# Optimization experiments

Hardware: AMD Instinct MI355X
Metric: run time of the kernel (lower is better)

## Reference

```python
import jax, jax.numpy as jnp
import numpy as np

N_NODES = 100000
N_EDGES = 1600000
IN_FEATS = 128
OUT_FEATS = 128


def setup_inputs() -> dict:
    key = jax.random.key(0)
    k1, k2, k3, k4, k5 = jax.random.split(key, 5)
    feature = jax.random.normal(k1, (N_NODES, IN_FEATS), dtype=jnp.float32)
    src = jax.random.randint(k2, (N_EDGES,), 0, N_NODES, dtype=jnp.int64)
    dst = jax.random.randint(k3, (N_EDGES,), 0, N_NODES, dtype=jnp.int64)
    # nn.Linear default init: U(-1/sqrt(in), 1/sqrt(in)); randn scaled is fine for a numeric baseline
    bound = 1.0 / np.sqrt(IN_FEATS)
    W = jax.random.uniform(k4, (OUT_FEATS, IN_FEATS), dtype=jnp.float32, minval=-bound, maxval=bound)
    b = jax.random.uniform(k5, (OUT_FEATS,), dtype=jnp.float32, minval=-bound, maxval=bound)
    return {"feature": feature, "src": src, "dst": dst, "W": W, "b": b}


def reference(feature, src, dst, W, b):
    # message passing: copy source feature along each edge, sum into destination node
    agg = jax.ops.segment_sum(feature[src], dst, num_segments=N_NODES)  # [N, in_feats]
    # node apply: ReLU(Linear(h))
    return jax.nn.relu(agg @ W.T + b)  # [N, out_feats]
```

## Files before the change

kernel.cpp:

```cpp
#include <hip/hip_runtime.h>

#define N_NODES 100000
#define N_EDGES 1600000
#define F 128

#define NB    1563
#define NBP2  2048
#define CAP   1280
#define CHUNK 8192

#define BIN_BLOCKS   196
#define HGEMM_BLOCKS 782
#define FRONT_GRID_LIN (BIN_BLOCKS + HGEMM_BLOCKS)

#define LDP  136
#define SMEM_BYTES 77824

typedef __bf16  bf16x8 __attribute__((ext_vector_type(8)));
typedef float   f32x4  __attribute__((ext_vector_type(4)));

__device__ inline unsigned short f32_to_bf16(float f) {
    unsigned u = __builtin_bit_cast(unsigned, f);
    u += 0x7FFFu + ((u >> 16) & 1u);
    return (unsigned short)(u >> 16);
}
__device__ inline unsigned pack_bf16x2(float lo, float hi) {
    return (unsigned)f32_to_bf16(lo) | ((unsigned)f32_to_bf16(hi) << 16);
}
__device__ inline void addrow(float* acc, const uint4 v) {
    acc[0] += __builtin_bit_cast(float, v.x << 16);
    acc[1] += __builtin_bit_cast(float, v.x & 0xFFFF0000u);
    acc[2] += __builtin_bit_cast(float, v.y << 16);
    acc[3] += __builtin_bit_cast(float, v.y & 0xFFFF0000u);
    acc[4] += __builtin_bit_cast(float, v.z << 16);
    acc[5] += __builtin_bit_cast(float, v.z & 0xFFFF0000u);
    acc[6] += __builtin_bit_cast(float, v.w << 16);
    acc[7] += __builtin_bit_cast(float, v.w & 0xFFFF0000u);
}

__global__ __launch_bounds__(1024) void gcn_front_lin(
    const float* __restrict__ feat, const float* __restrict__ W,
    const int* __restrict__ src, const int* __restrict__ dst,
    int* __restrict__ gcur, unsigned* __restrict__ bins,
    unsigned short* __restrict__ H)
{
    __shared__ __align__(16) unsigned char smem[SMEM_BYTES];

    const int tid = threadIdx.x;
    const int bx  = blockIdx.x;

    if (bx >= BIN_BLOCKS) {
        unsigned short* Alds = (unsigned short*)smem;
        unsigned short* Wlds = Alds + 128 * LDP;
        const int row0 = (bx - BIN_BLOCKS) * 128;

        #pragma unroll
        for (int i = 0; i < 4; ++i) {
            const int c = tid + i * 1024;
            const int r = c >> 5, cc = c & 31;
            const float4 v = *(const float4*)(W + (size_t)c * 4);
            uint2 p; p.x = pack_bf16x2(v.x, v.y); p.y = pack_bf16x2(v.z, v.w);
            *(uint2*)&Wlds[r * LDP + cc * 4] = p;
        }
        #pragma unroll
        for (int i = 0; i < 4; ++i) {
            const int c = tid + i * 1024;
            const int r = c >> 5, cc = c & 31;
            int gr = row0 + r; if (gr > N_NODES - 1) gr = N_NODES - 1;
            const float4 v = *(const float4*)(feat + (size_t)gr * F + cc * 4);
            uint2 p; p.x = pack_bf16x2(v.x, v.y); p.y = pack_bf16x2(v.z, v.w);
            *(uint2*)&Alds[r * LDP + cc * 4] = p;
        }
        __syncthreads();

        const int lane = tid & 63, wv = tid >> 6;
        const int lr = lane & 15, lq = lane >> 4;
        const int wr = wv & 7;
        const int wc = wv >> 3;

        f32x4 acc[4] = {};
        #pragma unroll
        for (int kk = 0; kk < 4; ++kk) {
            const bf16x8 a = __builtin_bit_cast(bf16x8,
                *(const uint4*)&Alds[(wr * 16 + lr) * LDP + kk * 32 + lq * 8]);
            #pragma unroll
            for (int n2 = 0; n2 < 4; ++n2) {
                const bf16x8 w = __builtin_bit_cast(bf16x8,
                    *(const uint4*)&Wlds[((wc * 4 + n2) * 16 + lr) * LDP + kk * 32 + lq * 8]);
                acc[n2] = __builtin_amdgcn_mfma_f32_16x16x32_bf16(a, w, acc[n2], 0, 0, 0);
            }
        }
        #pragma unroll
        for (int rg = 0; rg < 4; ++rg) {
            const int gr = row0 + wr * 16 + lq * 4 + rg;
            if (gr < N_NODES) {
                unsigned short* hrow = H + (size_t)gr * F;
                #pragma unroll
                for (int n2 = 0; n2 < 4; ++n2)
                    hrow[(wc * 4 + n2) * 16 + lr] = f32_to_bf16(acc[n2][rg]);
            }
        }
        return;
    }

    unsigned*       cnt    = (unsigned*)smem;
    unsigned*       off    = cnt + NBP2;
    int*            gbase  = (int*)(off + NBP2);
    unsigned*       staged = (unsigned*)(gbase + NBP2);
    unsigned short* sbk    = (unsigned short*)(staged + CHUNK);
    unsigned*       scan   = (unsigned*)(sbk + CHUNK);

    const int e0 = bx * CHUNK;

    #pragma unroll
    for (int i = 0; i < 2; ++i) cnt[tid + i * 1024] = 0;
    __syncthreads();

    int sv[8], dv[8];
    #pragma unroll
    for (int i = 0; i < 8; ++i) {
        const int e = e0 + tid + i * 1024;
        if (e < N_EDGES) {
            sv[i] = src[e];
            dv[i] = dst[e];
            atomicAdd(&cnt[dv[i] >> 6], 1u);
        } else dv[i] = -1;
    }
    __syncthreads();

    const unsigned s = cnt[2 * tid] + cnt[2 * tid + 1];
    scan[tid] = s;
    __syncthreads();
    for (int o = 1; o < 1024; o <<= 1) {
        const unsigned t = (tid >= o) ? scan[tid - o] : 0;
        __syncthreads();
        scan[tid] += t;
        __syncthreads();
    }
    const unsigned run = scan[tid] - s;
    off[2 * tid]     = run;
    off[2 * tid + 1] = run + cnt[2 * tid];
    __syncthreads();

    #pragma unroll
    for (int i = 0; i < 8; ++i) {
        if (dv[i] >= 0) {
            const int bk = dv[i] >> 6;
            const unsigned w = (unsigned)sv[i] | ((unsigned)(dv[i] & 63) << 17);
            const unsigned p = atomicAdd(&off[bk], 1u);
            staged[p] = w;
            sbk[p] = (unsigned short)bk;
        }
    }
    __syncthreads();

    #pragma unroll
    for (int i = 0; i < 2; ++i) {
        const int bk = 2 * tid + i;
        if (bk < NB && cnt[bk] > 0)
            gbase[bk] = atomicAdd(&gcur[bk], (int)cnt[bk]);
    }
    __syncthreads();

    const int c_tot = (int)scan[1023];
    for (int p = tid; p < c_tot; p += 1024) {
        const int bk = sbk[p];
        const int gp = gbase[bk] + (p - (int)(off[bk] - cnt[bk]));
        if (gp < CAP) bins[(size_t)bk * CAP + gp] = staged[p];
    }
}

__global__ __launch_bounds__(512) void gcn_accum_lin(
    const int* __restrict__ gcur,
    const unsigned* __restrict__ bins,
    const unsigned short* __restrict__ H,
    const float* __restrict__ b,
    float* __restrict__ out)
{
    __shared__ unsigned tmp[CAP];
    __shared__ unsigned list[CAP];
    __shared__ int cnt64[64], scn[64], pos64[64], cur64[64];

    const int tid = threadIdx.x;
    const int bkt = blockIdx.x;

    int c = gcur[bkt]; if (c > CAP) c = CAP;
    const unsigned* bb = bins + (size_t)bkt * CAP;

    for (int i = tid; i < c; i += 512) tmp[i] = bb[i];
    if (tid < 64) cnt64[tid] = 0;
    __syncthreads();

    for (int i = tid; i < c; i += 512) atomicAdd(&cnt64[(tmp[i] >> 17) & 63], 1);
    __syncthreads();

    if (tid < 64) scn[tid] = cnt64[tid];
    __syncthreads();
    #pragma unroll
    for (int o = 1; o < 64; o <<= 1) {
        int t = 0;
        if (tid < 64 && tid >= o) t = scn[tid - o];
        __syncthreads();
        if (tid < 64) scn[tid] += t;
        __syncthreads();
    }
    if (tid < 64) {
        const int st = scn[tid] - cnt64[tid];
        pos64[tid] = st;
        cur64[tid] = st;
    }
    __syncthreads();

    for (int i = tid; i < c; i += 512) {
        const unsigned w = tmp[i];
        const int p = atomicAdd(&cur64[(w >> 17) & 63], 1);
        list[p] = w;
    }
    __syncthreads();

    const int grp = tid >> 4;
    const int sl  = tid & 15;
    const int n0  = bkt * 64;

    #pragma unroll
    for (int ni = 0; ni < 2; ++ni) {
        const int l  = grp * 2 + ni;
        const int st = pos64[l];
        const int en = st + cnt64[l];

        float a0[8] = {0,0,0,0,0,0,0,0};
        float a1[8] = {0,0,0,0,0,0,0,0};
        int k = st;
        for (; k + 7 < en; k += 8) {
            const unsigned w0 = list[k],     w1 = list[k + 1];
            const unsigned w2 = list[k + 2], w3 = list[k + 3];
            const unsigned w4 = list[k + 4], w5 = list[k + 5];
            const unsigned w6 = list[k + 6], w7 = list[k + 7];
            const uint4 v0 = *(const uint4*)(H + (size_t)(w0 & 0x1FFFF) * F + sl * 8);
            const uint4 v1 = *(const uint4*)(H + (size_t)(w1 & 0x1FFFF) * F + sl * 8);
            const uint4 v2 = *(const uint4*)(H + (size_t)(w2 & 0x1FFFF) * F + sl * 8);
            const uint4 v3 = *(const uint4*)(H + (size_t)(w3 & 0x1FFFF) * F + sl * 8);
            const uint4 v4 = *(const uint4*)(H + (size_t)(w4 & 0x1FFFF) * F + sl * 8);
            const uint4 v5 = *(const uint4*)(H + (size_t)(w5 & 0x1FFFF) * F + sl * 8);
            const uint4 v6 = *(const uint4*)(H + (size_t)(w6 & 0x1FFFF) * F + sl * 8);
            const uint4 v7 = *(const uint4*)(H + (size_t)(w7 & 0x1FFFF) * F + sl * 8);
            addrow(a0, v0); addrow(a1, v1); addrow(a0, v2); addrow(a1, v3);
            addrow(a0, v4); addrow(a1, v5); addrow(a0, v6); addrow(a1, v7);
        }
        for (; k + 3 < en; k += 4) {
            const unsigned w0 = list[k],     w1 = list[k + 1];
            const unsigned w2 = list[k + 2], w3 = list[k + 3];
            const uint4 v0 = *(const uint4*)(H + (size_t)(w0 & 0x1FFFF) * F + sl * 8);
            const uint4 v1 = *(const uint4*)(H + (size_t)(w1 & 0x1FFFF) * F + sl * 8);
            const uint4 v2 = *(const uint4*)(H + (size_t)(w2 & 0x1FFFF) * F + sl * 8);
            const uint4 v3 = *(const uint4*)(H + (size_t)(w3 & 0x1FFFF) * F + sl * 8);
            addrow(a0, v0); addrow(a1, v1); addrow(a0, v2); addrow(a1, v3);
        }
        for (; k < en; ++k) {
            const unsigned w0 = list[k];
            const uint4 v0 = *(const uint4*)(H + (size_t)(w0 & 0x1FFFF) * F + sl * 8);
            addrow(a0, v0);
        }
        #pragma unroll
        for (int q = 0; q < 8; ++q) a0[q] += a1[q];

        const int n = n0 + l;
        if (n < N_NODES) {
            const float4 b0 = *(const float4*)(b + sl * 8);
            const float4 b1 = *(const float4*)(b + sl * 8 + 4);
            float4 o0, o1;
            o0.x = fmaxf(a0[0] + b0.x, 0.0f);
            o0.y = fmaxf(a0[1] + b0.y, 0.0f);
            o0.z = fmaxf(a0[2] + b0.z, 0.0f);
            o0.w = fmaxf(a0[3] + b0.w, 0.0f);
            o1.x = fmaxf(a0[4] + b1.x, 0.0f);
            o1.y = fmaxf(a0[5] + b1.y, 0.0f);
            o1.z = fmaxf(a0[6] + b1.z, 0.0f);
            o1.w = fmaxf(a0[7] + b1.w, 0.0f);
            float* orow = out + (size_t)n * F + sl * 8;
            *(float4*)orow = o0;
            *(float4*)(orow + 4) = o1;
        }
    }
}

#define FEAT_BLOCKS 3125
#define WCONV_BLOCKS 16
#define FRONT_GRID  (BIN_BLOCKS + FEAT_BLOCKS + WCONV_BLOCKS)

__global__ __launch_bounds__(1024) void gcn_front(
    const float* __restrict__ feat, const float* __restrict__ W,
    const int* __restrict__ src, const int* __restrict__ dst,
    int* __restrict__ gcur, unsigned* __restrict__ bins,
    unsigned short* __restrict__ Wbf, float* __restrict__ out)
{
    __shared__ unsigned cnt[NBP2];
    __shared__ unsigned off[NBP2];
    __shared__ int      gbase[NBP2];
    __shared__ unsigned staged[CHUNK];
    __shared__ unsigned short sbk[CHUNK];
    __shared__ unsigned scan[1024];

    const int tid = threadIdx.x;
    const int bx  = blockIdx.x;

    if (bx >= BIN_BLOCKS) {
        const int rb = bx - BIN_BLOCKS;
        if (rb < FEAT_BLOCKS) {
            const int t = rb * 1024 + tid;
            const float4 v = *(const float4*)(feat + (size_t)t * 4);
            uint2 p;
            p.x = pack_bf16x2(v.x, v.y);
            p.y = pack_bf16x2(v.z, v.w);
            const int n = t >> 5, q = t & 31;
            *(uint2*)((char*)out + (size_t)n * 512 + q * 8) = p;
        } else {
            const int i = (rb - FEAT_BLOCKS) * 1024 + tid;
            Wbf[i] = f32_to_bf16(W[i]);
        }
        return;
    }

    const int e0 = bx * CHUNK;

    #pragma unroll
    for (int i = 0; i < 2; ++i) cnt[tid + i * 1024] = 0;
    __syncthreads();

    int sv[8], dv[8];
    #pragma unroll
    for (int i = 0; i < 8; ++i) {
        const int e = e0 + tid + i * 1024;
        if (e < N_EDGES) {
            sv[i] = src[e];
            dv[i] = dst[e];
            atomicAdd(&cnt[dv[i] >> 6], 1u);
        } else dv[i] = -1;
    }
    __syncthreads();

    const unsigned s = cnt[2 * tid] + cnt[2 * tid + 1];
    scan[tid] = s;
    __syncthreads();
    for (int o = 1; o < 1024; o <<= 1) {
        const unsigned t = (tid >= o) ? scan[tid - o] : 0;
        __syncthreads();
        scan[tid] += t;
        __syncthreads();
    }
    const unsigned run = scan[tid] - s;
    off[2 * tid]     = run;
    off[2 * tid + 1] = run + cnt[2 * tid];
    __syncthreads();

    #pragma unroll
    for (int i = 0; i < 8; ++i) {
        if (dv[i] >= 0) {
            const int bk = dv[i] >> 6;
            const unsigned w = (unsigned)sv[i] | ((unsigned)(dv[i] & 63) << 17);
            const unsigned p = atomicAdd(&off[bk], 1u);
            staged[p] = w;
            sbk[p] = (unsigned short)bk;
        }
    }
    __syncthreads();

    #pragma unroll
    for (int i = 0; i < 2; ++i) {
        const int bk = 2 * tid + i;
        if (bk < NB && cnt[bk] > 0)
            gbase[bk] = atomicAdd(&gcur[bk], (int)cnt[bk]);
    }
    __syncthreads();

    const int c_tot = (int)scan[1023];
    for (int p = tid; p < c_tot; p += 1024) {
        const int bk = sbk[p];
        const int gp = gbase[bk] + (p - (int)(off[bk] - cnt[bk]));
        if (gp < CAP) bins[(size_t)bk * CAP + gp] = staged[p];
    }
}

__global__ __launch_bounds__(512) void gcn_accum2(
    const int* __restrict__ gcur,
    const unsigned* __restrict__ bins,
    float* __restrict__ out)
{
    __shared__ unsigned tmp[CAP];
    __shared__ unsigned list[CAP];
    __shared__ int cnt64[64], scn[64], pos64[64], cur64[64];

    const int tid = threadIdx.x;
    const int bkt = blockIdx.x;

    int c = gcur[bkt]; if (c > CAP) c = CAP;
    const unsigned* bb = bins + (size_t)bkt * CAP;

    for (int i = tid; i < c; i += 512) tmp[i] = bb[i];
    if (tid < 64) cnt64[tid] = 0;
    __syncthreads();

    for (int i = tid; i < c; i += 512) atomicAdd(&cnt64[(tmp[i] >> 17) & 63], 1);
    __syncthreads();

    if (tid < 64) scn[tid] = cnt64[tid];
    __syncthreads();
    #pragma unroll
    for (int o = 1; o < 64; o <<= 1) {
        int t = 0;
        if (tid < 64 && tid >= o) t = scn[tid - o];
        __syncthreads();
        if (tid < 64) scn[tid] += t;
        __syncthreads();
    }
    if (tid < 64) {
        const int st = scn[tid] - cnt64[tid];
        pos64[tid] = st;
        cur64[tid] = st;
    }
    __syncthreads();

    for (int i = tid; i < c; i += 512) {
        const unsigned w = tmp[i];
        const int p = atomicAdd(&cur64[(w >> 17) & 63], 1);
        list[p] = w;
    }
    __syncthreads();

    const int grp = tid >> 4;
    const int sl  = tid & 15;
    const int n0  = bkt * 64;

    #pragma unroll
    for (int ni = 0; ni < 2; ++ni) {
        const int l  = grp * 2 + ni;
        const int st = pos64[l];
        const int en = st + cnt64[l];

        float a0[8] = {0,0,0,0,0,0,0,0};
        float a1[8] = {0,0,0,0,0,0,0,0};
        int k = st;
        for (; k + 3 < en; k += 4) {
            const unsigned w0 = list[k],     w1 = list[k + 1];
            const unsigned w2 = list[k + 2], w3 = list[k + 3];
            const uint4 v0 = *(const uint4*)((const char*)out + (size_t)(w0 & 0x1FFFF) * 512 + sl * 16);
            const uint4 v1 = *(const uint4*)((const char*)out + (size_t)(w1 & 0x1FFFF) * 512 + sl * 16);
            const uint4 v2 = *(const uint4*)((const char*)out + (size_t)(w2 & 0x1FFFF) * 512 + sl * 16);
            const uint4 v3 = *(const uint4*)((const char*)out + (size_t)(w3 & 0x1FFFF) * 512 + sl * 16);
            addrow(a0, v0); addrow(a1, v1); addrow(a0, v2); addrow(a1, v3);
        }
        for (; k < en; ++k) {
            const unsigned w0 = list[k];
            const uint4 v0 = *(const uint4*)((const char*)out + (size_t)(w0 & 0x1FFFF) * 512 + sl * 16);
            addrow(a0, v0);
        }
        #pragma unroll
        for (int q = 0; q < 8; ++q) a0[q] += a1[q];

        const int n = n0 + l;
        if (n < N_NODES) {
            uint4 o;
            o.x = pack_bf16x2(a0[0], a0[1]);
            o.y = pack_bf16x2(a0[2], a0[3]);
            o.z = pack_bf16x2(a0[4], a0[5]);
            o.w = pack_bf16x2(a0[6], a0[7]);
            *(uint4*)((char*)out + (size_t)n * 512 + 256 + sl * 16) = o;
        }
    }
}

#define MT   128

__global__ __launch_bounds__(256) void gcn_gemm_mfma(
    float* __restrict__ out,
    const unsigned short* __restrict__ Wbf,
    const float* __restrict__ b)
{
    __shared__ unsigned short Alds[MT * LDP];
    __shared__ unsigned short Wlds[F * LDP];

    const int tid  = threadIdx.x;
    const int row0 = blockIdx.x * MT;

    #pragma unroll
    for (int i = 0; i < 8; ++i) {
        const int c = tid + i * 256;
        const int r = c >> 4, cc = c & 15;
        *(uint4*)&Wlds[r * LDP + cc * 8] = *(const uint4*)&Wbf[c * 8];
    }
    #pragma unroll
    for (int i = 0; i < 8; ++i) {
        const int c = tid + i * 256;
        const int r = c >> 4, cc = c & 15;
        int gr = row0 + r; if (gr > N_NODES - 1) gr = N_NODES - 1;
        const uint4 v = *(const uint4*)((const char*)out + (size_t)gr * 512 + 256 + cc * 16);
        *(uint4*)&Alds[r * LDP + cc * 8] = v;
    }
    __syncthreads();

    const int lane = tid & 63;
    const int wv   = tid >> 6;
    const int lr   = lane & 15;
    const int lq   = lane >> 4;

    f32x4 acc[2][8] = {};
    #pragma unroll
    for (int kk = 0; kk < 4; ++kk) {
        bf16x8 a[2], w[8];
        #pragma unroll
        for (int i = 0; i < 2; ++i)
            a[i] = __builtin_bit_cast(bf16x8,
                *(const uint4*)&Alds[(wv * 32 + i * 16 + lr) * LDP + kk * 32 + lq * 8]);
        #pragma unroll
        for (int n = 0; n < 8; ++n)
            w[n] = __builtin_bit_cast(bf16x8,
                *(const uint4*)&Wlds[(n * 16 + lr) * LDP + kk * 32 + lq * 8]);
        #pragma unroll
        for (int i = 0; i < 2; ++i)
            #pragma unroll
            for (int n = 0; n < 8; ++n)
                acc[i][n] = __builtin_amdgcn_mfma_f32_16x16x32_bf16(a[i], w[n], acc[i][n], 0, 0, 0);
    }

    float bias[8];
    #pragma unroll
    for (int n = 0; n < 8; ++n) bias[n] = b[n * 16 + lr];

    #pragma unroll
    for (int i = 0; i < 2; ++i) {
        const int rbase = wv * 32 + i * 16 + lq * 4;
        #pragma unroll
        for (int rg = 0; rg < 4; ++rg) {
            const int gr = row0 + rbase + rg;
            if (gr < N_NODES) {
                float* orow = out + (size_t)gr * F;
                #pragma unroll
                for (int n = 0; n < 8; ++n) {
                    const float v = acc[i][n][rg] + bias[n];
                    orow[n * 16 + lr] = v > 0.0f ? v : 0.0f;
                }
            }
        }
    }
}

__global__ __launch_bounds__(256) void gcn_scatter(
    const float* __restrict__ feat,
    const int* __restrict__ src, const int* __restrict__ dst,
    float* __restrict__ agg)
{
    const int sub  = threadIdx.x >> 5;
    const int lane = threadIdx.x & 31;
    const long long e = (long long)blockIdx.x * 8 + sub;
    if (e >= N_EDGES) return;
    const int s = src[e], d = dst[e];
    const float4 v = *(const float4*)(feat + (size_t)s * F + lane * 4);
    float* ar = agg + (size_t)d * F + lane * 4;
    unsafeAtomicAdd(ar + 0, v.x);
    unsafeAtomicAdd(ar + 1, v.y);
    unsafeAtomicAdd(ar + 2, v.z);
    unsafeAtomicAdd(ar + 3, v.w);
}

#define GR  64
#define LDW 132
__global__ __launch_bounds__(256) void gcn_gemm_relu(
    float* __restrict__ agg_out,
    const float* __restrict__ W, const float* __restrict__ b)
{
    __shared__ float Wl[F][LDW];
    __shared__ float At[GR][LDW];
    const int tid = threadIdx.x;
    const long long row0 = (long long)blockIdx.x * GR;
    #pragma unroll
    for (int i = 0; i < 64; ++i) {
        const int e = tid + i * 256;
        Wl[e >> 7][e & 127] = W[e];
    }
    #pragma unroll
    for (int i = 0; i < 32; ++i) {
        const int e = tid + i * 256;
        const int r = e >> 7, k2 = e & 127;
        const long long gr = row0 + r;
        At[r][k2] = (gr < N_NODES) ? agg_out[gr * F + k2] : 0.0f;
    }
    __syncthreads();
    const int tx = tid & 15, ty = tid >> 4, r0 = ty * 4;
    float acc[4][8];
    #pragma unroll
    for (int r = 0; r < 4; ++r)
        #pragma unroll
        for (int m = 0; m < 8; ++m) acc[r][m] = 0.0f;
    for (int k0 = 0; k0 < F; k0 += 4) {
        float4 a[4], w[8];
        #pragma unroll
        for (int r = 0; r < 4; ++r) a[r] = *(const float4*)&At[r0 + r][k0];
        #pragma unroll
        for (int m = 0; m < 8; ++m) w[m] = *(const float4*)&Wl[tx + 16 * m][k0];
        #pragma unroll
        for (int r = 0; r < 4; ++r)
            #pragma unroll
            for (int m = 0; m < 8; ++m)
                acc[r][m] += a[r].x * w[m].x + a[r].y * w[m].y
                           + a[r].z * w[m].z + a[r].w * w[m].w;
    }
    float bias[8];
    #pragma unroll
    for (int m = 0; m < 8; ++m) bias[m] = b[tx + 16 * m];
    __syncthreads();
    #pragma unroll
    for (int r = 0; r < 4; ++r) {
        const long long gr = row0 + r0 + r;
        if (gr < N_NODES) {
            float* orow = agg_out + gr * F;
            #pragma unroll
            for (int m = 0; m < 8; ++m) {
                const float v = acc[r][m] + bias[m];
                orow[tx + 16 * m] = v > 0.0f ? v : 0.0f;
            }
        }
    }
}

extern "C" void kernel_launch(void* const* d_in, const int* in_sizes, int n_in,
                              void* d_out, int out_size, void* d_ws, size_t ws_size,
                              hipStream_t stream) {
    const float* feat = (const float*)d_in[0];
    const int*   src  = (const int*)d_in[1];
    const int*   dst  = (const int*)d_in[2];
    const float* W    = (const float*)d_in[3];
    const float* b    = (const float*)d_in[4];
    float* out = (float*)d_out;

    const size_t ws_lin = 1600u * 4 + (size_t)NB * CAP * 4 + (size_t)N_NODES * F * 2;
    const size_t ws_old = 1600u * 4 + (size_t)NB * CAP * 4 + (size_t)F * F * 2;

    if (ws_size >= ws_lin) {
        int* gcur = (int*)d_ws;
        unsigned* bins = (unsigned*)(gcur + 1600);
        unsigned short* H = (unsigned short*)(bins + (size_t)NB * CAP);

        hipMemsetAsync(gcur, 0, NB * sizeof(int), stream);
        gcn_front_lin<<<FRONT_GRID_LIN, 1024, 0, stream>>>(feat, W, src, dst, gcur, bins, H);
        gcn_accum_lin<<<NB, 512, 0, stream>>>(gcur, bins, H, b, out);
    } else if (ws_size >= ws_old) {
        int* gcur = (int*)d_ws;
        unsigned* bins = (unsigned*)(gcur + 1600);
        unsigned short* Wbf = (unsigned short*)(bins + (size_t)NB * CAP);

        hipMemsetAsync(gcur, 0, NB * sizeof(int), stream);
        gcn_front   <<<FRONT_GRID, 1024, 0, stream>>>(feat, W, src, dst, gcur, bins, Wbf, out);
        gcn_accum2  <<<NB, 512, 0, stream>>>(gcur, bins, out);
        gcn_gemm_mfma<<<(N_NODES + MT - 1) / MT, 256, 0, stream>>>(out, Wbf, b);
    } else {
        hipMemsetAsync(out, 0, (size_t)N_NODES * F * sizeof(float), stream);
        gcn_scatter<<<N_EDGES / 8, 256, 0, stream>>>(feat, src, dst, out);
        gcn_gemm_relu<<<(N_NODES + GR - 1) / GR, 256, 0, stream>>>(out, W, b);
    }
}
```

Measured before the change: 191.4 us.

## Pre-convert W once, coalesce H stores, use wave-shuffle scan, dynamic node scheduling

Several independent changes land together. A small init kernel now converts W to bf16 once and zeroes the bin counters, replacing the memset, so the GEMM blocks no longer each convert W from fp32. The H tile is staged through LDS so it can be written as coalesced 16-byte rows instead of scattered 2-byte stores. The 1024-element block scan becomes a two-level wave-shuffle scan with far fewer barriers. The accumulate kernel hands out nodes to 16-thread groups through an LDS atomic counter to balance uneven degrees. This adds one kernel launch and a larger workspace requirement, which could push execution onto a fallback path.

```diff
diff --git a/kernel.cpp b/kernel.cpp
--- a/kernel.cpp
+++ b/kernel.cpp
@@ -38,8 +38,17 @@
     acc[7] += __builtin_bit_cast(float, v.w & 0xFFFF0000u);
 }
 
+__global__ __launch_bounds__(1024) void gcn_init(
+    const float* __restrict__ W, unsigned short* __restrict__ Wbf,
+    int* __restrict__ gcur)
+{
+    const int i = blockIdx.x * 1024 + threadIdx.x;
+    Wbf[i] = f32_to_bf16(W[i]);
+    if (i < 1600) gcur[i] = 0;
+}
+
 __global__ __launch_bounds__(1024) void gcn_front_lin(
-    const float* __restrict__ feat, const float* __restrict__ W,
+    const float* __restrict__ feat, const unsigned short* __restrict__ Wbf,
     const int* __restrict__ src, const int* __restrict__ dst,
     int* __restrict__ gcur, unsigned* __restrict__ bins,
     unsigned short* __restrict__ H)
@@ -55,12 +64,10 @@
         const int row0 = (bx - BIN_BLOCKS) * 128;
 
         #pragma unroll
-        for (int i = 0; i < 4; ++i) {
+        for (int i = 0; i < 2; ++i) {
             const int c = tid + i * 1024;
-            const int r = c >> 5, cc = c & 31;
-            const float4 v = *(const float4*)(W + (size_t)c * 4);
-            uint2 p; p.x = pack_bf16x2(v.x, v.y); p.y = pack_bf16x2(v.z, v.w);
-            *(uint2*)&Wlds[r * LDP + cc * 4] = p;
+            const int r = c >> 4, cc = c & 15;
+            *(uint4*)&Wlds[r * LDP + cc * 8] = *(const uint4*)&Wbf[c * 8];
         }
         #pragma unroll
         for (int i = 0; i < 4; ++i) {
@@ -90,15 +97,24 @@
                 acc[n2] = __builtin_amdgcn_mfma_f32_16x16x32_bf16(a, w, acc[n2], 0, 0, 0);
             }
         }
+        __syncthreads();
+
         #pragma unroll
         for (int rg = 0; rg < 4; ++rg) {
-            const int gr = row0 + wr * 16 + lq * 4 + rg;
-            if (gr < N_NODES) {
-                unsigned short* hrow = H + (size_t)gr * F;
-                #pragma unroll
-                for (int n2 = 0; n2 < 4; ++n2)
-                    hrow[(wc * 4 + n2) * 16 + lr] = f32_to_bf16(acc[n2][rg]);
-            }
+            const int r = wr * 16 + lq * 4 + rg;
+            #pragma unroll
+            for (int n2 = 0; n2 < 4; ++n2)
+                Alds[r * LDP + (wc * 4 + n2) * 16 + lr] = f32_to_bf16(acc[n2][rg]);
+        }
+        __syncthreads();
+
+        #pragma unroll
+        for (int i = 0; i < 2; ++i) {
+            const int c = tid + i * 1024;
+            const int r = c >> 4, cc = c & 15;
+            const int gr = row0 + r;
+            if (gr < N_NODES)
+                *(uint4*)(H + (size_t)gr * F + cc * 8) = *(const uint4*)&Alds[r * LDP + cc * 8];
         }
         return;
     }
@@ -128,16 +144,30 @@
     }
     __syncthreads();
 
+    const int lane = tid & 63, wid = tid >> 6;
     const unsigned s = cnt[2 * tid] + cnt[2 * tid + 1];
-    scan[tid] = s;
-    __syncthreads();
-    for (int o = 1; o < 1024; o <<= 1) {
-        const unsigned t = (tid >= o) ? scan[tid - o] : 0;
-        __syncthreads();
-        scan[tid] += t;
-        __syncthreads();
-    }
-    const unsigned run = scan[tid] - s;
+    unsigned v = s;
+    #pragma unroll
+    for (int o = 1; o < 64; o <<= 1) {
+        const unsigned t = __shfl_up(v, o, 64);
+        if (lane >= o) v += t;
+    }
+    if (lane == 63) scan[wid] = v;
+    __syncthreads();
+    if (tid < 16) {
+        const unsigned w = scan[tid];
+        unsigned x = w;
+        #pragma unroll
+        for (int o = 1; o < 16; o <<= 1) {
+            const unsigned t = __shfl_up(x, o, 16);
+            if (tid >= o) x += t;
+        }
+        scan[tid] = x - w;
+        if (tid == 15) scan[16] = x;
+    }
+    __syncthreads();
+    const unsigned incl = v + scan[wid];
+    const unsigned run  = incl - s;
     off[2 * tid]     = run;
     off[2 * tid + 1] = run + cnt[2 * tid];
     __syncthreads();
@@ -162,7 +192,7 @@
     }
     __syncthreads();
 
-    const int c_tot = (int)scan[1023];
+    const int c_tot = (int)scan[16];
     for (int p = tid; p < c_tot; p += 1024) {
         const int bk = sbk[p];
         const int gp = gbase[bk] + (p - (int)(off[bk] - cnt[bk]));
@@ -180,6 +210,7 @@
     __shared__ unsigned tmp[CAP];
     __shared__ unsigned list[CAP];
     __shared__ int cnt64[64], scn[64], pos64[64], cur64[64];
+    __shared__ int nextn;
 
     const int tid = threadIdx.x;
     const int bkt = blockIdx.x;
@@ -209,6 +240,7 @@
         pos64[tid] = st;
         cur64[tid] = st;
     }
+    if (tid == 0) nextn = 0;
     __syncthreads();
 
     for (int i = tid; i < c; i += 512) {
@@ -218,15 +250,19 @@
     }
     __syncthreads();
 
-    const int grp = tid >> 4;
-    const int sl  = tid & 15;
-    const int n0  = bkt * 64;
-
-    #pragma unroll
-    for (int ni = 0; ni < 2; ++ni) {
-        const int l  = grp * 2 + ni;
-        const int st = pos64[l];
-        const int en = st + cnt64[l];
+    const int grp  = tid >> 4;
+    const int sl   = tid & 15;
+    const int lane = tid & 63;
+    const int n0   = bkt * 64;
+
+    for (;;) {
+        int myn = 0;
+        if (sl == 0) myn = atomicAdd(&nextn, 1);
+        myn = __shfl(myn, lane & 48, 64);
+        if (myn >= 64) break;
+
+        const int st = pos64[myn];
+        const int en = st + cnt64[myn];
 
         float a0[8] = {0,0,0,0,0,0,0,0};
         float a1[8] = {0,0,0,0,0,0,0,0};
@@ -264,7 +300,7 @@
         #pragma unroll
         for (int q = 0; q < 8; ++q) a0[q] += a1[q];
 
-        const int n = n0 + l;
+        const int n = n0 + myn;
         if (n < N_NODES) {
             const float4 b0 = *(const float4*)(b + sl * 8);
             const float4 b1 = *(const float4*)(b + sl * 8 + 4);
@@ -632,16 +668,18 @@
     const float* b    = (const float*)d_in[4];
     float* out = (float*)d_out;
 
-    const size_t ws_lin = 1600u * 4 + (size_t)NB * CAP * 4 + (size_t)N_NODES * F * 2;
+    const size_t ws_lin = 1600u * 4 + (size_t)NB * CAP * 4
+                        + (size_t)N_NODES * F * 2 + (size_t)F * F * 2;
     const size_t ws_old = 1600u * 4 + (size_t)NB * CAP * 4 + (size_t)F * F * 2;
 
     if (ws_size >= ws_lin) {
         int* gcur = (int*)d_ws;
         unsigned* bins = (unsigned*)(gcur + 1600);
         unsigned short* H = (unsigned short*)(bins + (size_t)NB * CAP);
-
-        hipMemsetAsync(gcur, 0, NB * sizeof(int), stream);
-        gcn_front_lin<<<FRONT_GRID_LIN, 1024, 0, stream>>>(feat, W, src, dst, gcur, bins, H);
+        unsigned short* Wbf = H + (size_t)N_NODES * F;
+
+        gcn_init     <<<16, 1024, 0, stream>>>(W, Wbf, gcur);
+        gcn_front_lin<<<FRONT_GRID_LIN, 1024, 0, stream>>>(feat, Wbf, src, dst, gcur, bins, H);
         gcn_accum_lin<<<NB, 512, 0, stream>>>(gcur, bins, H, b, out);
     } else if (ws_size >= ws_old) {
         int* gcur = (int*)d_ws;
```

Result: faster. 187.4 us (-2.1%).
